# Optimization experiments

Hardware: AMD Instinct MI355X
Metric: run time of the kernel (lower is better)

The kernel has to match this reference:

```python
import math
import jax, jax.numpy as jnp
import numpy as np

B, T, D, H = 8, 2048, 1024, 32  # batch, positions, feature_dim, max_history (==T_hist)
DECAY_RATE = 0.95


def setup_inputs() -> dict:
    key = jax.random.key(0)
    ks = jax.random.split(key, 10)
    s = 1.0 / math.sqrt(D)
    inp = {
        "x": jax.random.normal(ks[0], (B, T, D), jnp.float32),
        "history": jax.random.normal(ks[1], (T, H, D), jnp.float32),  # [P=T, T_hist, D]
        "Wq": jax.random.normal(ks[2], (D, D), jnp.float32) * s,
        "bq": jnp.zeros((D,), jnp.float32),
        "Wk": jax.random.normal(ks[3], (D, D), jnp.float32) * s,
        "bk": jnp.zeros((D,), jnp.float32),
        "Wv": jax.random.normal(ks[4], (D, D), jnp.float32) * s,
        "bv": jnp.zeros((D,), jnp.float32),
        "Wo": jax.random.normal(ks[5], (D, D), jnp.float32) * s,
        "bo": jnp.zeros((D,), jnp.float32),
        "decay": jnp.asarray(DECAY_RATE ** np.arange(H), jnp.float32),
    }
    return inp


def reference(x, history, Wq, bq, Wk, bk, Wv, bv, Wo, bo, decay):
    # x: [B,T,D]; history: [T,T_hist,D]
    d = x.shape[-1]
    t_hist = history.shape[1]
    Q = x @ Wq.T + bq                       # [B,T,D]
    K = history @ Wk.T + bk                 # [T,T_hist,D]
    V = history @ Wv.T + bv                 # [T,T_hist,D]
    # per-position scores: Q[b,t,:] . K[t,h,:]
    scores = jnp.einsum('btd,thd->bth', Q, K) / jnp.sqrt(jnp.asarray(d, x.dtype))
    bias = jnp.log(decay[:t_hist][::-1] + 1e-10)  # [T_hist] (flipped, oldest gets smallest weight)
    attn = jax.nn.softmax(scores + bias, axis=-1)  # [B,T,T_hist]
    attended = jnp.einsum('bth,thd->btd', attn, V)  # [B,T,D]
    return (attended + x) @ Wo.T + bo
```

## Files before the change

kernel.cpp:

```cpp
#include <hip/hip_runtime.h>


#define BB 8
#define TT 2048
#define DD 1024
#define HH 32

typedef __attribute__((ext_vector_type(8))) short short8;
typedef __attribute__((ext_vector_type(4))) float f32x4;

__device__ __forceinline__ short f2b(float f) {
  unsigned u = __float_as_uint(f);
  unsigned r = u + 0x7fffu + ((u >> 16) & 1u);
  return (short)(r >> 16);
}

__device__ __forceinline__ void gload_lds16(const void* g, void* l) {
  __builtin_amdgcn_global_load_lds(
      (const __attribute__((address_space(1))) void*)g,
      (__attribute__((address_space(3))) void*)l, 16, 0, 0);
}

__global__ void k_transpose3(const float* __restrict__ Wq, const float* __restrict__ Wk,
                             const float* __restrict__ Wv,
                             short* __restrict__ WqT, short* __restrict__ WkT,
                             short* __restrict__ WvT) {
  __shared__ float tile[32][33];
  const float* src = blockIdx.z == 0 ? Wq : (blockIdx.z == 1 ? Wk : Wv);
  short* dst = blockIdx.z == 0 ? WqT : (blockIdx.z == 1 ? WkT : WvT);
  const int bx = blockIdx.x * 32, by = blockIdx.y * 32;
  const int tx = threadIdx.x, ty = threadIdx.y;
#pragma unroll
  for (int k = 0; k < 4; k++)
    tile[ty + 8 * k][tx] = src[(size_t)(by + ty + 8 * k) * DD + bx + tx];
  __syncthreads();
#pragma unroll
  for (int k = 0; k < 4; k++)
    dst[(size_t)(bx + ty + 8 * k) * DD + by + tx] = f2b(tile[tx][ty + 8 * k]);
}

__global__ void k_conv_right(const float* __restrict__ src, short* __restrict__ dst) {
  size_t i = ((size_t)blockIdx.x * 256 + threadIdx.x) * 8;
  float4 a = *(const float4*)(src + i);
  float4 b = *(const float4*)(src + i + 4);
  short8 o;
  o[0] = f2b(a.x); o[1] = f2b(a.y); o[2] = f2b(a.z); o[3] = f2b(a.w);
  o[4] = f2b(b.x); o[5] = f2b(b.y); o[6] = f2b(b.z); o[7] = f2b(b.w);
  size_t r = i >> 10, c = i & 1023;
  *(short8*)(dst + r * 2048 + 1024 + c) = o;
}

__global__ void k_u3(const float* __restrict__ Wk, const float* __restrict__ bq,
                     float* __restrict__ u3) {
  const int d = blockIdx.x * 256 + threadIdx.x;
  float a0 = 0, a1 = 0, a2 = 0, a3 = 0, a4 = 0, a5 = 0, a6 = 0, a7 = 0;
  for (int j = 0; j < DD; j += 8) {
    a0 = fmaf(Wk[(size_t)(j + 0) * DD + d], bq[j + 0], a0);
    a1 = fmaf(Wk[(size_t)(j + 1) * DD + d], bq[j + 1], a1);
    a2 = fmaf(Wk[(size_t)(j + 2) * DD + d], bq[j + 2], a2);
    a3 = fmaf(Wk[(size_t)(j + 3) * DD + d], bq[j + 3], a3);
    a4 = fmaf(Wk[(size_t)(j + 4) * DD + d], bq[j + 4], a4);
    a5 = fmaf(Wk[(size_t)(j + 5) * DD + d], bq[j + 5], a5);
    a6 = fmaf(Wk[(size_t)(j + 6) * DD + d], bq[j + 6], a6);
    a7 = fmaf(Wk[(size_t)(j + 7) * DD + d], bq[j + 7], a7);
  }
  u3[d] = ((a0 + a1) + (a2 + a3)) + ((a4 + a5) + (a6 + a7));
}

__global__ void k_bfinal(const float* __restrict__ Wo, const float* __restrict__ bvv,
                         const float* __restrict__ bo, float* __restrict__ bf) {
  const int j = blockIdx.x;
  const int tid = threadIdx.x;
  float acc = 0.f;
  for (int d = tid; d < DD; d += 256) acc = fmaf(Wo[(size_t)j * DD + d], bvv[d], acc);
#pragma unroll
  for (int off = 32; off >= 1; off >>= 1) acc += __shfl_down(acc, off);
  __shared__ float p[4];
  if ((tid & 63) == 0) p[tid >> 6] = acc;
  __syncthreads();
  if (tid == 0) bf[j] = p[0] + p[1] + p[2] + p[3] + bo[j];
}

__global__ __launch_bounds__(256) void k_gemm64x2(const short* __restrict__ WkT,
                                                  const short* __restrict__ WqT,
                                                  short* __restrict__ A2,
                                                  const short* __restrict__ WoB,
                                                  const short* __restrict__ WvT,
                                                  short* __restrict__ WB) {
  __shared__ short At[64 * 32];
  __shared__ short Bt[64 * 32];
  const short* A; const short* B; short* C; int lda, ldb, ldc;
  if (blockIdx.z == 0) {
    A = WkT; lda = 1024; B = WqT; ldb = 1024; C = A2; ldc = 1024;
  } else {
    A = WoB; lda = 2048; B = WvT; ldb = 1024; C = WB; ldc = 2048;
  }
  const int tid = threadIdx.x;
  const int w = tid >> 6, l = tid & 63;
  const int wm = w >> 1, wn = w & 1;
  const int lrow = l & 15, lk = l >> 4;
  const size_t m0 = (size_t)blockIdx.x * 64;
  const size_t n0 = (size_t)blockIdx.y * 64;

  f32x4 acc[2][2];
#pragma unroll
  for (int i = 0; i < 2; i++)
#pragma unroll
    for (int j = 0; j < 2; j++) acc[i][j] = (f32x4){0.f, 0.f, 0.f, 0.f};

  const unsigned ubase = (unsigned)((tid & ~63) * 16);
  const int r0 = tid >> 2, kc = tid & 3;

  for (int k0 = 0; k0 < 1024; k0 += 32) {
    __syncthreads();
    gload_lds16(A + (m0 + r0) * lda + k0 + kc * 8, (char*)At + ubase);
    gload_lds16(B + (n0 + r0) * ldb + k0 + kc * 8, (char*)Bt + ubase);
    __syncthreads();
    short8 af[2], bfv[2];
    const int aoff = (wm * 32 + lrow) * 32 + lk * 8;
    const int boff = (wn * 32 + lrow) * 32 + lk * 8;
#pragma unroll
    for (int mi = 0; mi < 2; mi++) af[mi] = *(const short8*)(At + aoff + mi * 512);
#pragma unroll
    for (int ni = 0; ni < 2; ni++) bfv[ni] = *(const short8*)(Bt + boff + ni * 512);
#pragma unroll
    for (int mi = 0; mi < 2; mi++)
#pragma unroll
      for (int ni = 0; ni < 2; ni++)
        acc[mi][ni] = __builtin_amdgcn_mfma_f32_16x16x32_bf16(af[mi], bfv[ni],
                                                              acc[mi][ni], 0, 0, 0);
  }

#pragma unroll
  for (int ni = 0; ni < 2; ni++) {
    const size_t col = n0 + wn * 32 + ni * 16 + lrow;
#pragma unroll
    for (int mi = 0; mi < 2; mi++) {
#pragma unroll
      for (int q = 0; q < 4; q++) {
        const size_t row = m0 + wm * 32 + mi * 16 + lk * 4 + q;
        C[row * ldc + col] = f2b(acc[mi][ni][q]);
      }
    }
  }
}

template <bool OUT_BF16>
__global__ __launch_bounds__(512) void k_gemm256(const short* __restrict__ A, int lda,
                                                 const short* __restrict__ B, int ldb,
                                                 void* __restrict__ Cv, int ldc, int K,
                                                 const float* __restrict__ bias,
                                                 int mblocks) {
  extern __shared__ char lds[];
  const int tid = threadIdx.x;
  const int w = tid >> 6;
  const int l = tid & 63;
  const int wm = w >> 2, wn = w & 3;
  const int lrow = l & 15, lk = l >> 4;

  const int nwg = gridDim.x;
  const int cpx = nwg >> 3;
  const int lin = blockIdx.x;
  const int wg = (lin & 7) * cpx + (lin >> 3);
  const int mb = wg % mblocks;
  const int nb = wg / mblocks;
  const size_t m0 = (size_t)mb * 256;
  const size_t n0 = (size_t)nb * 256;

  const int r0 = tid >> 3;
  const int r1 = 64 + (tid >> 3);
  const int kk0 = (((tid & 7) * 16) ^ (((tid >> 5) & 1) << 5)) >> 1;
  const short* pA00 = A + (m0 + r0) * lda + kk0;
  const short* pA01 = A + (m0 + r1) * lda + kk0;
  const short* pA10 = A + (m0 + 128 + r0) * lda + kk0;
  const short* pA11 = A + (m0 + 128 + r1) * lda + kk0;
  const short* pB00 = B + (n0 + r0) * ldb + kk0;
  const short* pB01 = B + (n0 + r1) * ldb + kk0;
  const short* pB10 = B + (n0 + 128 + r0) * ldb + kk0;
  const short* pB11 = B + (n0 + 128 + r1) * ldb + kk0;
  const unsigned wb16 = (unsigned)((tid & ~63) * 16);

  f32x4 acc[8][4];
#pragma unroll
  for (int i = 0; i < 8; i++)
#pragma unroll
    for (int j = 0; j < 4; j++) acc[i][j] = (f32x4){0.f, 0.f, 0.f, 0.f};

  const int NT = K >> 6;

#define STAGE256(bufsel, koff)                                    \
  do {                                                            \
    char* ab_ = lds + (bufsel) * 32768;                           \
    char* bb_ = lds + 65536 + (bufsel) * 32768;                   \
    gload_lds16(pA00 + (koff), ab_ + wb16);                       \
    gload_lds16(pA01 + (koff), ab_ + 8192 + wb16);                \
    gload_lds16(pA10 + (koff), ab_ + 16384 + wb16);               \
    gload_lds16(pA11 + (koff), ab_ + 24576 + wb16);               \
    gload_lds16(pB00 + (koff), bb_ + wb16);                       \
    gload_lds16(pB01 + (koff), bb_ + 8192 + wb16);                \
    gload_lds16(pB10 + (koff), bb_ + 16384 + wb16);               \
    gload_lds16(pB11 + (koff), bb_ + 24576 + wb16);               \
  } while (0)

  STAGE256(0, 0);
  asm volatile("s_waitcnt vmcnt(0)" ::: "memory");
  __syncthreads();

  const int aswz = ((lrow >> 2) & 1) << 5;

  for (int kt = 0; kt < NT; ++kt) {
    const int cur = kt & 1;
    const char* Ab = lds + cur * 32768 + wm * 16384;
    const char* Bb = lds + 65536 + cur * 32768 + (wn >> 1) * 16384;
    const int bro = (wn & 1) * 64;

    short8 bfr[4][2];
#pragma unroll
    for (int fn = 0; fn < 4; fn++)
#pragma unroll
      for (int ks = 0; ks < 2; ks++) {
        const int ph = (((bro + fn * 16 + lrow) * 128 + ks * 64 + lk * 16)) ^ aswz;
        bfr[fn][ks] = *(const short8*)(Bb + ph);
      }

#pragma unroll
    for (int p = 0; p < 4; p++) {
      short8 af[2][2];
#pragma unroll
      for (int rr = 0; rr < 2; rr++)
#pragma unroll
        for (int ks = 0; ks < 2; ks++) {
          const int ph =
              ((((p * 2 + rr) * 16 + lrow) * 128 + ks * 64 + lk * 16)) ^ aswz;
          af[rr][ks] = *(const short8*)(Ab + ph);
        }
      if (p == 0 && kt + 1 < NT) STAGE256(1 - cur, (size_t)(kt + 1) * 64);
      __builtin_amdgcn_s_barrier();
      __builtin_amdgcn_sched_barrier(0);
      __builtin_amdgcn_s_setprio(1);
#pragma unroll
      for (int ks = 0; ks < 2; ks++)
#pragma unroll
        for (int rr = 0; rr < 2; rr++)
#pragma unroll
          for (int fn = 0; fn < 4; fn++)
            acc[p * 2 + rr][fn] = __builtin_amdgcn_mfma_f32_16x16x32_bf16(
                af[rr][ks], bfr[fn][ks], acc[p * 2 + rr][fn], 0, 0, 0);
      __builtin_amdgcn_s_setprio(0);
      __builtin_amdgcn_s_barrier();
      __builtin_amdgcn_sched_barrier(0);
    }
    asm volatile("s_waitcnt vmcnt(0)" ::: "memory");
    __builtin_amdgcn_s_barrier();
    __builtin_amdgcn_sched_barrier(0);
  }
#undef STAGE256

#pragma unroll
  for (int fn = 0; fn < 4; fn++) {
    const size_t col = n0 + wn * 64 + fn * 16 + lrow;
    const float bv_ = bias ? bias[col] : 0.f;
#pragma unroll
    for (int fr = 0; fr < 8; fr++) {
#pragma unroll
      for (int q = 0; q < 4; q++) {
        const size_t row = m0 + wm * 128 + fr * 16 + lk * 4 + q;
        const float v = acc[fr][fn][q] + bv_;
        if (OUT_BF16)
          ((short*)Cv)[row * ldc + col] = f2b(v);
        else
          ((float*)Cv)[row * ldc + col] = v;
      }
    }
  }
}

__global__ __launch_bounds__(512) void k_fused(const short* __restrict__ xA,
                                               const float* __restrict__ hist,
                                               const float* __restrict__ u3,
                                               const float* __restrict__ decay,
                                               short* __restrict__ CC) {
  extern __shared__ char smem[];
  short* histT = (short*)smem;
  float* spart = (float*)(smem + 65536);
  float* sfull = (float*)(smem + 65536 + 8192);
  short* attnb = (short*)(smem + 65536 + 8192 + 2048);

  const int t = blockIdx.x;
  const int tid = threadIdx.x;
  const int w = tid >> 6, l = tid & 63;
  const int lrow = l & 15, lk = l >> 4;

  f32x4 accs[2];
  accs[0] = (f32x4){0.f, 0.f, 0.f, 0.f};
  accs[1] = (f32x4){0.f, 0.f, 0.f, 0.f};

#pragma unroll
  for (int kk = 0; kk < 4; kk++) {
    const int ka = (w * 4 + kk) * 32 + lk * 8;
    short8 af;
    if (lrow < 8) {
      af = *(const short8*)(xA + ((size_t)lrow * TT + t) * DD + ka);
    } else if (lrow == 8) {
      const float* up = u3 + ka;
#pragma unroll
      for (int j = 0; j < 8; j++) af[j] = f2b(up[j]);
    } else {
#pragma unroll
      for (int j = 0; j < 8; j++) af[j] = 0;
    }
#pragma unroll
    for (int nt = 0; nt < 2; nt++) {
      const int h = lrow + nt * 16;
      const float* hp = hist + ((size_t)t * HH + h) * DD + ka;
      float4 h0 = *(const float4*)hp;
      float4 h1 = *(const float4*)(hp + 4);
      short8 bv_;
      bv_[0] = f2b(h0.x); bv_[1] = f2b(h0.y); bv_[2] = f2b(h0.z); bv_[3] = f2b(h0.w);
      bv_[4] = f2b(h1.x); bv_[5] = f2b(h1.y); bv_[6] = f2b(h1.z); bv_[7] = f2b(h1.w);
      accs[nt] = __builtin_amdgcn_mfma_f32_16x16x32_bf16(af, bv_, accs[nt], 0, 0, 0);
      const int hs = h >> 3, hl = h & 7;
#pragma unroll
      for (int j = 0; j < 8; j++) {
        const int d = ka + j;
        histT[(d << 5) + ((hs ^ ((d >> 1) & 3)) << 3) + hl] = bv_[j];
      }
    }
  }

  for (int half = 4; half >= 1; half >>= 1) {
    __syncthreads();
    if (w >= half && w < 2 * half) {
#pragma unroll
      for (int nt = 0; nt < 2; nt++)
#pragma unroll
        for (int q = 0; q < 4; q++)
          spart[(w - half) * 512 + (lk * 4 + q) * 32 + nt * 16 + lrow] = accs[nt][q];
    }
    __syncthreads();
    if (w < half) {
#pragma unroll
      for (int nt = 0; nt < 2; nt++)
#pragma unroll
        for (int q = 0; q < 4; q++)
          accs[nt][q] += spart[w * 512 + (lk * 4 + q) * 32 + nt * 16 + lrow];
    }
  }
  if (w == 0) {
#pragma unroll
    for (int nt = 0; nt < 2; nt++)
#pragma unroll
      for (int q = 0; q < 4; q++)
        sfull[(lk * 4 + q) * 32 + nt * 16 + lrow] = accs[nt][q];
  }
  __syncthreads();

  {
    const int bb = tid >> 5, h = tid & 31;
    float s = (sfull[bb * 32 + h] + sfull[8 * 32 + h]) * (1.0f / 32.0f) +
              logf(decay[31 - h] + 1e-10f);
    float m = s;
#pragma unroll
    for (int msk = 16; msk >= 1; msk >>= 1) m = fmaxf(m, __shfl_xor(m, msk));
    float p = expf(s - m);
    float den = p;
#pragma unroll
    for (int msk = 16; msk >= 1; msk >>= 1) den += __shfl_xor(den, msk);
    attnb[bb * 32 + h] = f2b(p / den);
  }
  __syncthreads();

  short8 paf = *(const short8*)(attnb + lrow * 32 + lk * 8);
  const f32x4 z4 = (f32x4){0.f, 0.f, 0.f, 0.f};
#pragma unroll
  for (int i = 0; i < 8; i++) {
    const int d0 = (w * 8 + i) * 16;
    const int d = d0 + lrow;
    short8 hb = *(const short8*)(histT + (d << 5) + ((lk ^ ((d >> 1) & 3)) << 3));
    f32x4 o = __builtin_amdgcn_mfma_f32_16x16x32_bf16(paf, hb, z4, 0, 0, 0);
    if (lk < 2) {
#pragma unroll
      for (int q = 0; q < 4; q++) {
        const int b = lk * 4 + q;
        CC[((size_t)b * TT + t) * 2048 + d0 + lrow] = f2b(o[q]);
      }
    }
  }
}

extern "C" void kernel_launch(void* const* d_in, const int* in_sizes, int n_in,
                              void* d_out, int out_size, void* d_ws, size_t ws_size,
                              hipStream_t stream) {
  (void)in_sizes; (void)n_in; (void)out_size; (void)ws_size;
  const float* x    = (const float*)d_in[0];
  const float* hist = (const float*)d_in[1];
  const float* Wq   = (const float*)d_in[2];
  const float* bq   = (const float*)d_in[3];
  const float* Wk   = (const float*)d_in[4];
  const float* Wv   = (const float*)d_in[6];
  const float* bv   = (const float*)d_in[7];
  const float* Wo   = (const float*)d_in[8];
  const float* bo   = (const float*)d_in[9];
  const float* dec  = (const float*)d_in[10];
  float* out = (float*)d_out;
  char* ws = (char*)d_ws;

  short* CC   = (short*)(ws + 0);
  short* xA   = (short*)(ws + 67108864);
  short* A2   = (short*)(ws + 100663296);
  short* WB   = (short*)(ws + 102760448);
  short* WqT  = (short*)(ws + 106954752);
  short* WkT  = (short*)(ws + 109051904);
  short* WvT  = (short*)(ws + 111149056);
  float* bfin = (float*)(ws + 113246208);
  float* u3   = (float*)(ws + 113250304);

  hipFuncSetAttribute((const void*)k_fused, hipFuncAttributeMaxDynamicSharedMemorySize,
                      76800);
  hipFuncSetAttribute((const void*)k_gemm256<true>,
                      hipFuncAttributeMaxDynamicSharedMemorySize, 131072);
  hipFuncSetAttribute((const void*)k_gemm256<false>,
                      hipFuncAttributeMaxDynamicSharedMemorySize, 131072);

  k_transpose3<<<dim3(32, 32, 3), dim3(32, 8), 0, stream>>>(Wq, Wk, Wv, WqT, WkT, WvT);
  k_conv_right<<<8192, 256, 0, stream>>>(x, CC);
  k_conv_right<<<512, 256, 0, stream>>>(Wo, WB);
  k_u3<<<4, 256, 0, stream>>>(Wk, bq, u3);
  k_bfinal<<<1024, 256, 0, stream>>>(Wo, bv, bo, bfin);
  k_gemm64x2<<<dim3(16, 16, 2), 256, 0, stream>>>(WkT, WqT, A2, WB + 1024, WvT, WB);
  k_gemm256<true><<<256, 512, 131072, stream>>>(CC + 1024, 2048, A2, 1024, xA, 1024,
                                                1024, nullptr, 64);
  k_fused<<<2048, 512, 76800, stream>>>(xA, hist, u3, dec, CC);
  k_gemm256<false><<<256, 512, 131072, stream>>>(CC, 2048, WB, 2048, out, 1024, 2048,
                                                 bfin, 64);
}
```

Measured before the change: 300.3 us.

## Merge five prep kernels into one launch and remap GEMM tile order

Result: faster. 288.1 us (-4.1%).

```diff
diff --git a/kernel.cpp b/kernel.cpp
--- a/kernel.cpp
+++ b/kernel.cpp
@@ -21,64 +21,63 @@
       (__attribute__((address_space(3))) void*)l, 16, 0, 0);
 }
 
-__global__ void k_transpose3(const float* __restrict__ Wq, const float* __restrict__ Wk,
-                             const float* __restrict__ Wv,
-                             short* __restrict__ WqT, short* __restrict__ WkT,
-                             short* __restrict__ WvT) {
-  __shared__ float tile[32][33];
-  const float* src = blockIdx.z == 0 ? Wq : (blockIdx.z == 1 ? Wk : Wv);
-  short* dst = blockIdx.z == 0 ? WqT : (blockIdx.z == 1 ? WkT : WvT);
-  const int bx = blockIdx.x * 32, by = blockIdx.y * 32;
-  const int tx = threadIdx.x, ty = threadIdx.y;
-#pragma unroll
-  for (int k = 0; k < 4; k++)
-    tile[ty + 8 * k][tx] = src[(size_t)(by + ty + 8 * k) * DD + bx + tx];
-  __syncthreads();
-#pragma unroll
-  for (int k = 0; k < 4; k++)
-    dst[(size_t)(bx + ty + 8 * k) * DD + by + tx] = f2b(tile[tx][ty + 8 * k]);
-}
-
-__global__ void k_conv_right(const float* __restrict__ src, short* __restrict__ dst) {
-  size_t i = ((size_t)blockIdx.x * 256 + threadIdx.x) * 8;
-  float4 a = *(const float4*)(src + i);
-  float4 b = *(const float4*)(src + i + 4);
-  short8 o;
-  o[0] = f2b(a.x); o[1] = f2b(a.y); o[2] = f2b(a.z); o[3] = f2b(a.w);
-  o[4] = f2b(b.x); o[5] = f2b(b.y); o[6] = f2b(b.z); o[7] = f2b(b.w);
-  size_t r = i >> 10, c = i & 1023;
-  *(short8*)(dst + r * 2048 + 1024 + c) = o;
-}
-
-__global__ void k_u3(const float* __restrict__ Wk, const float* __restrict__ bq,
-                     float* __restrict__ u3) {
-  const int d = blockIdx.x * 256 + threadIdx.x;
-  float a0 = 0, a1 = 0, a2 = 0, a3 = 0, a4 = 0, a5 = 0, a6 = 0, a7 = 0;
-  for (int j = 0; j < DD; j += 8) {
-    a0 = fmaf(Wk[(size_t)(j + 0) * DD + d], bq[j + 0], a0);
-    a1 = fmaf(Wk[(size_t)(j + 1) * DD + d], bq[j + 1], a1);
-    a2 = fmaf(Wk[(size_t)(j + 2) * DD + d], bq[j + 2], a2);
-    a3 = fmaf(Wk[(size_t)(j + 3) * DD + d], bq[j + 3], a3);
-    a4 = fmaf(Wk[(size_t)(j + 4) * DD + d], bq[j + 4], a4);
-    a5 = fmaf(Wk[(size_t)(j + 5) * DD + d], bq[j + 5], a5);
-    a6 = fmaf(Wk[(size_t)(j + 6) * DD + d], bq[j + 6], a6);
-    a7 = fmaf(Wk[(size_t)(j + 7) * DD + d], bq[j + 7], a7);
-  }
-  u3[d] = ((a0 + a1) + (a2 + a3)) + ((a4 + a5) + (a6 + a7));
-}
-
-__global__ void k_bfinal(const float* __restrict__ Wo, const float* __restrict__ bvv,
-                         const float* __restrict__ bo, float* __restrict__ bf) {
-  const int j = blockIdx.x;
+__global__ __launch_bounds__(256) void k_prep(
+    const float* __restrict__ x, const float* __restrict__ Wq,
+    const float* __restrict__ bq, const float* __restrict__ Wk,
+    const float* __restrict__ Wv, const float* __restrict__ bv,
+    const float* __restrict__ Wo, const float* __restrict__ bo,
+    short* __restrict__ WqT, short* __restrict__ WkT, short* __restrict__ WvT,
+    short* __restrict__ CC, short* __restrict__ WB, float* __restrict__ u3,
+    float* __restrict__ bfin) {
+  const int b = blockIdx.x;
   const int tid = threadIdx.x;
-  float acc = 0.f;
-  for (int d = tid; d < DD; d += 256) acc = fmaf(Wo[(size_t)j * DD + d], bvv[d], acc);
-#pragma unroll
-  for (int off = 32; off >= 1; off >>= 1) acc += __shfl_down(acc, off);
-  __shared__ float p[4];
-  if ((tid & 63) == 0) p[tid >> 6] = acc;
-  __syncthreads();
-  if (tid == 0) bf[j] = p[0] + p[1] + p[2] + p[3] + bo[j];
+  if (b < 3072) {
+    __shared__ float tile[32][33];
+    const int z = b >> 10, rem = b & 1023;
+    const float* src = z == 0 ? Wq : (z == 1 ? Wk : Wv);
+    short* dst = z == 0 ? WqT : (z == 1 ? WkT : WvT);
+    const int bx = (rem & 31) * 32, by = (rem >> 5) * 32;
+    const int tx = tid & 31, ty = tid >> 5;
+#pragma unroll
+    for (int k = 0; k < 4; k++)
+      tile[ty + 8 * k][tx] = src[(size_t)(by + ty + 8 * k) * DD + bx + tx];
+    __syncthreads();
+#pragma unroll
+    for (int k = 0; k < 4; k++)
+      dst[(size_t)(bx + ty + 8 * k) * DD + by + tx] = f2b(tile[tx][ty + 8 * k]);
+  } else if (b < 11776) {
+    const bool isx = b < 11264;
+    const float* src = isx ? x : Wo;
+    short* dst = isx ? CC : WB;
+    size_t i = (((size_t)(b - (isx ? 3072 : 11264))) * 256 + tid) * 8;
+    float4 a = *(const float4*)(src + i);
+    float4 c = *(const float4*)(src + i + 4);
+    short8 o;
+    o[0] = f2b(a.x); o[1] = f2b(a.y); o[2] = f2b(a.z); o[3] = f2b(a.w);
+    o[4] = f2b(c.x); o[5] = f2b(c.y); o[6] = f2b(c.z); o[7] = f2b(c.w);
+    size_t r = i >> 10, cc = i & 1023;
+    *(short8*)(dst + r * 2048 + 1024 + cc) = o;
+  } else if (b < 11780) {
+    const int d = (b - 11776) * 256 + tid;
+    float a0 = 0, a1 = 0, a2 = 0, a3 = 0;
+    for (int j = 0; j < DD; j += 4) {
+      a0 = fmaf(Wk[(size_t)(j + 0) * DD + d], bq[j + 0], a0);
+      a1 = fmaf(Wk[(size_t)(j + 1) * DD + d], bq[j + 1], a1);
+      a2 = fmaf(Wk[(size_t)(j + 2) * DD + d], bq[j + 2], a2);
+      a3 = fmaf(Wk[(size_t)(j + 3) * DD + d], bq[j + 3], a3);
+    }
+    u3[d] = (a0 + a1) + (a2 + a3);
+  } else {
+    const int j = b - 11780;
+    float acc = 0.f;
+    for (int d = tid; d < DD; d += 256) acc = fmaf(Wo[(size_t)j * DD + d], bv[d], acc);
+#pragma unroll
+    for (int off = 32; off >= 1; off >>= 1) acc += __shfl_down(acc, off);
+    __shared__ float p[4];
+    if ((tid & 63) == 0) p[tid >> 6] = acc;
+    __syncthreads();
+    if (tid == 0) bfin[j] = p[0] + p[1] + p[2] + p[3] + bo[j];
+  }
 }
 
 __global__ __launch_bounds__(256) void k_gemm64x2(const short* __restrict__ WkT,
@@ -150,7 +149,7 @@
                                                  const short* __restrict__ B, int ldb,
                                                  void* __restrict__ Cv, int ldc, int K,
                                                  const float* __restrict__ bias,
-                                                 int mblocks) {
+                                                 int nblocks) {
   extern __shared__ char lds[];
   const int tid = threadIdx.x;
   const int w = tid >> 6;
@@ -162,8 +161,8 @@
   const int cpx = nwg >> 3;
   const int lin = blockIdx.x;
   const int wg = (lin & 7) * cpx + (lin >> 3);
-  const int mb = wg % mblocks;
-  const int nb = wg / mblocks;
+  const int mb = wg / nblocks;
+  const int nb = wg % nblocks;
   const size_t m0 = (size_t)mb * 256;
   const size_t n0 = (size_t)nb * 256;
 
@@ -422,15 +421,12 @@
   hipFuncSetAttribute((const void*)k_gemm256<false>,
                       hipFuncAttributeMaxDynamicSharedMemorySize, 131072);
 
-  k_transpose3<<<dim3(32, 32, 3), dim3(32, 8), 0, stream>>>(Wq, Wk, Wv, WqT, WkT, WvT);
-  k_conv_right<<<8192, 256, 0, stream>>>(x, CC);
-  k_conv_right<<<512, 256, 0, stream>>>(Wo, WB);
-  k_u3<<<4, 256, 0, stream>>>(Wk, bq, u3);
-  k_bfinal<<<1024, 256, 0, stream>>>(Wo, bv, bo, bfin);
+  k_prep<<<12804, 256, 0, stream>>>(x, Wq, bq, Wk, Wv, bv, Wo, bo, WqT, WkT, WvT, CC,
+                                    WB, u3, bfin);
   k_gemm64x2<<<dim3(16, 16, 2), 256, 0, stream>>>(WkT, WqT, A2, WB + 1024, WvT, WB);
   k_gemm256<true><<<256, 512, 131072, stream>>>(CC + 1024, 2048, A2, 1024, xA, 1024,
-                                                1024, nullptr, 64);
+                                                1024, nullptr, 4);
   k_fused<<<2048, 512, 76800, stream>>>(xA, hist, u3, dec, CC);
   k_gemm256<false><<<256, 512, 131072, stream>>>(CC, 2048, WB, 2048, out, 1024, 2048,
-                                                 bfin, 64);
-}
+                                                 bfin, 4);
+}
```
